# Optimization experiments

Measured on AMD Instinct MI355X. Metric: run time of the kernel, lower is better.

## Reference

```python
import jax, jax.numpy as jnp
import numpy as np

NUM_HEADS = 8
OUT_DIM = 32


def setup_inputs() -> dict:
    key = jax.random.key(0)
    k1, k2, k3, k4 = jax.random.split(key, 4)
    B, N, IN = 2048, 64, 256
    h_i_list = jax.random.normal(k1, (B, N, IN), dtype=jnp.float32)
    h_j_list = jax.random.normal(k2, (B, N, IN), dtype=jnp.float32)
    # Linear weight, applied as x @ W (in_dim, num_heads*out_dim)
    W = jax.random.normal(k3, (IN, NUM_HEADS * OUT_DIM), dtype=jnp.float32) * (1.0 / np.sqrt(IN))
    W_att = jax.random.normal(k4, (1, NUM_HEADS, OUT_DIM), dtype=jnp.float32) * 0.1
    return {"h_i_list": h_i_list, "h_j_list": h_j_list, "W": W, "W_att": W_att}


def reference(h_i_list, h_j_list, W, W_att):
    B, N, _ = h_i_list.shape
    H, D = NUM_HEADS, OUT_DIM
    # [B, N, H, D]
    proj_neigh = (h_j_list @ W).reshape(B, N, H, D)
    proj_self = (h_i_list @ W).reshape(B, N, H, D)
    # attention logits: leakyReLU(sum over feature dim) -> [B, N, H]
    e_ij = jax.nn.leaky_relu(((proj_neigh + proj_self) * W_att[None]).sum(-1), 0.2)
    # softmax over neighbor dim (dim=1)
    alpha = jax.nn.softmax(e_ij, axis=1)  # [B, N, H]
    # weighted neighbor sum -> [B, H, D]
    weight_sum = jnp.einsum("bnh,bnhd->bhd", alpha, proj_neigh)
    # concat=True: [B, 1, H*D]
    h_new = weight_sum.reshape(B, 1, H * D)
    return jax.nn.elu(h_new)
```

## Files before the change

### kernel.cpp

```cpp
#include <hip/hip_runtime.h>

#define NN 64
#define IND 256
#define NH 8
#define OD 32

__device__ __forceinline__ unsigned f2bf(float f) {
  unsigned u = __float_as_uint(f);
  return (u + (((u >> 16) & 1u) + 0x7fffu)) >> 16;
}
__device__ __forceinline__ float bflo(unsigned u) { return __uint_as_float(u << 16); }
__device__ __forceinline__ float bfhi(unsigned u) { return __uint_as_float(u & 0xffff0000u); }

__global__ __launch_bounds__(256) void precompute_v(
    const float* __restrict__ W, const float* __restrict__ Watt, float* __restrict__ V) {
  int tid = blockIdx.x * 256 + threadIdx.x;
  if (tid >= IND * NH) return;
  int h = tid >> 8, k = tid & 255;
  float acc = 0.f;
#pragma unroll
  for (int d = 0; d < OD; ++d) acc += W[k * 256 + h * OD + d] * Watt[h * OD + d];
  V[h * 256 + k] = acc;
}

#define V_OFF 33792
#define E_OFF (33792 + 8320)
#define M_OFF (33792 + 8320 + 2048)
#define SMEM_BYTES (33792 + 8320 + 2048 + 64)

__global__ __launch_bounds__(256) void gat_fused(
    const float* __restrict__ Xi, const float* __restrict__ Xj,
    const float* __restrict__ W, const float* __restrict__ V,
    float* __restrict__ out) {
  __shared__ __align__(16) unsigned char smem[SMEM_BYTES];
  unsigned* s_pk = (unsigned*)smem;
  float* v_f = (float*)(smem + V_OFF);
  float* e_f = (float*)(smem + E_OFF);
  float* m_f = (float*)(smem + M_OFF);
  float* r_f = m_f + 8;
  float* yp_f = (float*)smem;
  float* y_f = (float*)(smem + V_OFF);

  const int t = threadIdx.x;
  const int b = blockIdx.x;
  const int w = t >> 6, l = t & 63;
  const float4* Xi4 = (const float4*)Xi + (size_t)b * (NN * IND / 4);
  const float4* Xj4 = (const float4*)Xj + (size_t)b * (NN * IND / 4);

#pragma unroll
  for (int r = 0; r < 8; ++r) v_f[r * 260 + t] = V[r * 256 + t];

  float4 xj[16];
#pragma unroll
  for (int i = 0; i < 16; ++i) {
    int f4 = i * 256 + t;
    float4 a = Xj4[f4];
    float4 c = Xi4[f4];
    xj[i] = a;
    float sx = a.x + c.x, sy = a.y + c.y, sz = a.z + c.z, sw = a.w + c.w;
    int n = i * 4 + w;
    unsigned p0 = f2bf(sx) | (f2bf(sy) << 16);
    unsigned p1 = f2bf(sz) | (f2bf(sw) << 16);
    *(uint2*)(s_pk + n * 132 + l * 2) = make_uint2(p0, p1);
  }
  __syncthreads();

#pragma unroll
  for (int pp = 0; pp < 2; ++pp) {
    int p = t + pp * 256;
    int n = p >> 3, h = p & 7;
    const uint4* srow = (const uint4*)(s_pk + n * 132);
    const float4* vrow = (const float4*)(v_f + h * 260);
    float acc = 0.f;
#pragma unroll 8
    for (int kk = 0; kk < 32; ++kk) {
      uint4 sp = srow[kk];
      float4 va = vrow[2 * kk], vb = vrow[2 * kk + 1];
      acc += bflo(sp.x) * va.x + bfhi(sp.x) * va.y + bflo(sp.y) * va.z + bfhi(sp.y) * va.w
           + bflo(sp.z) * vb.x + bfhi(sp.z) * vb.y + bflo(sp.w) * vb.z + bfhi(sp.w) * vb.w;
    }
    e_f[p] = acc >= 0.f ? acc : 0.2f * acc;
  }
  __syncthreads();

  if (t < 64) {
    int h = t & 7, g = t >> 3;
    float m = -3.4e38f;
#pragma unroll
    for (int q = 0; q < 8; ++q) m = fmaxf(m, e_f[(g * 8 + q) * 8 + h]);
    m = fmaxf(m, __shfl_xor(m, 8, 64));
    m = fmaxf(m, __shfl_xor(m, 16, 64));
    m = fmaxf(m, __shfl_xor(m, 32, 64));
    float s = 0.f;
#pragma unroll
    for (int q = 0; q < 8; ++q) s += __expf(e_f[(g * 8 + q) * 8 + h] - m);
    s += __shfl_xor(s, 8, 64);
    s += __shfl_xor(s, 16, 64);
    s += __shfl_xor(s, 32, 64);
    if (g == 0) { m_f[h] = m; r_f[h] = 1.f / s; }
  }
  __syncthreads();

#pragma unroll
  for (int pp = 0; pp < 2; ++pp) {
    int p = t + pp * 256;
    int h = p & 7;
    e_f[p] = __expf(e_f[p] - m_f[h]) * r_f[h];
  }
  __syncthreads();

  float4 acc4[8];
#pragma unroll
  for (int h = 0; h < 8; ++h) acc4[h] = make_float4(0.f, 0.f, 0.f, 0.f);
#pragma unroll
  for (int i = 0; i < 16; ++i) {
    int n = i * 4 + w;
    float4 a0 = *(const float4*)(e_f + n * 8);
    float4 a1 = *(const float4*)(e_f + n * 8 + 4);
    float al[8] = {a0.x, a0.y, a0.z, a0.w, a1.x, a1.y, a1.z, a1.w};
    float4 x = xj[i];
#pragma unroll
    for (int h = 0; h < 8; ++h) {
      acc4[h].x += al[h] * x.x;
      acc4[h].y += al[h] * x.y;
      acc4[h].z += al[h] * x.z;
      acc4[h].w += al[h] * x.w;
    }
  }
#pragma unroll
  for (int h = 0; h < 8; ++h)
    *(float4*)(yp_f + (w * 8 + h) * 256 + l * 4) = acc4[h];
  __syncthreads();

#pragma unroll
  for (int r = 0; r < 8; ++r) {
    float y = yp_f[r * 256 + t] + yp_f[(8 + r) * 256 + t] +
              yp_f[(16 + r) * 256 + t] + yp_f[(24 + r) * 256 + t];
    y_f[r * 258 + t] = y;
  }
  __syncthreads();

  {
    int h = t >> 5;
    const float* yrow = y_f + h * 258;
    float acc = 0.f;
#pragma unroll 8
    for (int k = 0; k < 256; ++k) acc += yrow[k] * W[k * 256 + t];
    out[(size_t)b * 256 + t] = acc > 0.f ? acc : (__expf(acc) - 1.f);
  }
}

extern "C" void kernel_launch(void* const* d_in, const int* in_sizes, int n_in,
                              void* d_out, int out_size, void* d_ws, size_t ws_size,
                              hipStream_t stream) {
  const float* Xi = (const float*)d_in[0];
  const float* Xj = (const float*)d_in[1];
  const float* W = (const float*)d_in[2];
  const float* Watt = (const float*)d_in[3];
  float* out = (float*)d_out;
  float* V = (float*)d_ws;
  int B = in_sizes[0] / (NN * IND);
  precompute_v<<<(IND * NH + 255) / 256, 256, 0, stream>>>(W, Watt, V);
  gat_fused<<<B, 256, 0, stream>>>(Xi, Xj, W, V, out);
}
```

Measured before the change: 322.2 us.

## Restructure GAT fused kernel to cut barriers and split the output projection

Each wave now owns a contiguous block of 16 neighbor rows. All Xi/Xj float4 loads are issued before any packing, and the softmax statistics are computed redundantly in every wave with shuffles, which removes the m/r shared-memory stage and two block barriers. The final W projection is split along K across waves, using float4 W loads and a fused partial-sum reduction. A minimum-blocks hint of 3 is added to launch_bounds. Holding xi in registers raises register pressure, and the occupancy hint may force spills.

```diff
diff --git a/kernel.cpp b/kernel.cpp
--- a/kernel.cpp
+++ b/kernel.cpp
@@ -24,11 +24,10 @@
 }
 
 #define V_OFF 33792
-#define E_OFF (33792 + 8320)
-#define M_OFF (33792 + 8320 + 2048)
-#define SMEM_BYTES (33792 + 8320 + 2048 + 64)
+#define E_OFF (V_OFF + 8320)
+#define SMEM_BYTES (E_OFF + 2048)
 
-__global__ __launch_bounds__(256) void gat_fused(
+__global__ __launch_bounds__(256, 3) void gat_fused(
     const float* __restrict__ Xi, const float* __restrict__ Xj,
     const float* __restrict__ W, const float* __restrict__ V,
     float* __restrict__ out) {
@@ -36,39 +35,45 @@
   unsigned* s_pk = (unsigned*)smem;
   float* v_f = (float*)(smem + V_OFF);
   float* e_f = (float*)(smem + E_OFF);
-  float* m_f = (float*)(smem + M_OFF);
-  float* r_f = m_f + 8;
+  float* alpha_f = v_f;
+  float* pp_f = v_f;
   float* yp_f = (float*)smem;
-  float* y_f = (float*)(smem + V_OFF);
 
   const int t = threadIdx.x;
   const int b = blockIdx.x;
   const int w = t >> 6, l = t & 63;
-  const float4* Xi4 = (const float4*)Xi + (size_t)b * (NN * IND / 4);
-  const float4* Xj4 = (const float4*)Xj + (size_t)b * (NN * IND / 4);
+  const int g = l >> 3, h = l & 7;
 
+  const float4* Xi4 = (const float4*)Xi + (size_t)b * (NN * IND / 4) + w * 1024;
+  const float4* Xj4 = (const float4*)Xj + (size_t)b * (NN * IND / 4) + w * 1024;
+
+  {
+    const float4* V4 = (const float4*)V;
+    float4 vs[8];
 #pragma unroll
-  for (int r = 0; r < 8; ++r) v_f[r * 260 + t] = V[r * 256 + t];
+    for (int r = 0; r < 8; ++r) vs[r] = V4[r * 64 + l];
+#pragma unroll
+    for (int r = 0; r < 8; ++r) *(float4*)(v_f + r * 260 + 4 * l) = vs[r];
+  }
 
-  float4 xj[16];
+  float4 xj[16], xi[16];
 #pragma unroll
   for (int i = 0; i < 16; ++i) {
-    int f4 = i * 256 + t;
-    float4 a = Xj4[f4];
-    float4 c = Xi4[f4];
-    xj[i] = a;
-    float sx = a.x + c.x, sy = a.y + c.y, sz = a.z + c.z, sw = a.w + c.w;
-    int n = i * 4 + w;
-    unsigned p0 = f2bf(sx) | (f2bf(sy) << 16);
-    unsigned p1 = f2bf(sz) | (f2bf(sw) << 16);
-    *(uint2*)(s_pk + n * 132 + l * 2) = make_uint2(p0, p1);
+    xj[i] = Xj4[i * 64 + l];
+    xi[i] = Xi4[i * 64 + l];
   }
-  __syncthreads();
+#pragma unroll
+  for (int i = 0; i < 16; ++i) {
+    float4 a = xj[i], c = xi[i];
+    unsigned p0 = f2bf(a.x + c.x) | (f2bf(a.y + c.y) << 16);
+    unsigned p1 = f2bf(a.z + c.z) | (f2bf(a.w + c.w) << 16);
+    *(uint2*)(s_pk + (w * 16 + i) * 132 + l * 2) = make_uint2(p0, p1);
+  }
 
+  float er[2];
 #pragma unroll
   for (int pp = 0; pp < 2; ++pp) {
-    int p = t + pp * 256;
-    int n = p >> 3, h = p & 7;
+    int n = w * 16 + g + 8 * pp;
     const uint4* srow = (const uint4*)(s_pk + n * 132);
     const float4* vrow = (const float4*)(v_f + h * 260);
     float acc = 0.f;
@@ -79,74 +84,76 @@
       acc += bflo(sp.x) * va.x + bfhi(sp.x) * va.y + bflo(sp.y) * va.z + bfhi(sp.y) * va.w
            + bflo(sp.z) * vb.x + bfhi(sp.z) * vb.y + bflo(sp.w) * vb.z + bfhi(sp.w) * vb.w;
     }
-    e_f[p] = acc >= 0.f ? acc : 0.2f * acc;
+    er[pp] = acc >= 0.f ? acc : 0.2f * acc;
+    e_f[n * 8 + h] = er[pp];
   }
   __syncthreads();
 
-  if (t < 64) {
-    int h = t & 7, g = t >> 3;
-    float m = -3.4e38f;
+  float m = -3.4e38f;
 #pragma unroll
-    for (int q = 0; q < 8; ++q) m = fmaxf(m, e_f[(g * 8 + q) * 8 + h]);
-    m = fmaxf(m, __shfl_xor(m, 8, 64));
-    m = fmaxf(m, __shfl_xor(m, 16, 64));
-    m = fmaxf(m, __shfl_xor(m, 32, 64));
-    float s = 0.f;
+  for (int q = 0; q < 8; ++q) m = fmaxf(m, e_f[(g * 8 + q) * 8 + h]);
+  m = fmaxf(m, __shfl_xor(m, 8, 64));
+  m = fmaxf(m, __shfl_xor(m, 16, 64));
+  m = fmaxf(m, __shfl_xor(m, 32, 64));
+  float ssum = 0.f;
 #pragma unroll
-    for (int q = 0; q < 8; ++q) s += __expf(e_f[(g * 8 + q) * 8 + h] - m);
-    s += __shfl_xor(s, 8, 64);
-    s += __shfl_xor(s, 16, 64);
-    s += __shfl_xor(s, 32, 64);
-    if (g == 0) { m_f[h] = m; r_f[h] = 1.f / s; }
-  }
-  __syncthreads();
+  for (int q = 0; q < 8; ++q) ssum += __expf(e_f[(g * 8 + q) * 8 + h] - m);
+  ssum += __shfl_xor(ssum, 8, 64);
+  ssum += __shfl_xor(ssum, 16, 64);
+  ssum += __shfl_xor(ssum, 32, 64);
+  float rinv = 1.f / ssum;
 
 #pragma unroll
   for (int pp = 0; pp < 2; ++pp) {
-    int p = t + pp * 256;
-    int h = p & 7;
-    e_f[p] = __expf(e_f[p] - m_f[h]) * r_f[h];
+    int n = w * 16 + g + 8 * pp;
+    alpha_f[n * 8 + h] = __expf(er[pp] - m) * rinv;
   }
-  __syncthreads();
 
   float4 acc4[8];
 #pragma unroll
-  for (int h = 0; h < 8; ++h) acc4[h] = make_float4(0.f, 0.f, 0.f, 0.f);
+  for (int hh = 0; hh < 8; ++hh) acc4[hh] = make_float4(0.f, 0.f, 0.f, 0.f);
 #pragma unroll
   for (int i = 0; i < 16; ++i) {
-    int n = i * 4 + w;
-    float4 a0 = *(const float4*)(e_f + n * 8);
-    float4 a1 = *(const float4*)(e_f + n * 8 + 4);
+    int n = w * 16 + i;
+    float4 a0 = *(const float4*)(alpha_f + n * 8);
+    float4 a1 = *(const float4*)(alpha_f + n * 8 + 4);
     float al[8] = {a0.x, a0.y, a0.z, a0.w, a1.x, a1.y, a1.z, a1.w};
     float4 x = xj[i];
 #pragma unroll
-    for (int h = 0; h < 8; ++h) {
-      acc4[h].x += al[h] * x.x;
-      acc4[h].y += al[h] * x.y;
-      acc4[h].z += al[h] * x.z;
-      acc4[h].w += al[h] * x.w;
+    for (int hh = 0; hh < 8; ++hh) {
+      acc4[hh].x += al[hh] * x.x;
+      acc4[hh].y += al[hh] * x.y;
+      acc4[hh].z += al[hh] * x.z;
+      acc4[hh].w += al[hh] * x.w;
     }
   }
 #pragma unroll
-  for (int h = 0; h < 8; ++h)
-    *(float4*)(yp_f + (w * 8 + h) * 256 + l * 4) = acc4[h];
+  for (int hh = 0; hh < 8; ++hh)
+    *(float4*)(yp_f + (w * 8 + hh) * 260 + 4 * l) = acc4[hh];
   __syncthreads();
 
-#pragma unroll
-  for (int r = 0; r < 8; ++r) {
-    float y = yp_f[r * 256 + t] + yp_f[(8 + r) * 256 + t] +
-              yp_f[(16 + r) * 256 + t] + yp_f[(24 + r) * 256 + t];
-    y_f[r * 258 + t] = y;
+  {
+    const float* ypb = yp_f + g * 260;
+    const float4* W4 = (const float4*)W;
+    float4 acc = make_float4(0.f, 0.f, 0.f, 0.f);
+    int k0 = w * 64;
+#pragma unroll 8
+    for (int kk = 0; kk < 64; ++kk) {
+      int k = k0 + kk;
+      float yv = ypb[k] + ypb[2080 + k] + ypb[4160 + k] + ypb[6240 + k];
+      float4 wv = W4[k * 64 + l];
+      acc.x += yv * wv.x;
+      acc.y += yv * wv.y;
+      acc.z += yv * wv.z;
+      acc.w += yv * wv.w;
+    }
+    *(float4*)(pp_f + w * 256 + 4 * l) = acc;
   }
   __syncthreads();
 
   {
-    int h = t >> 5;
-    const float* yrow = y_f + h * 258;
-    float acc = 0.f;
-#pragma unroll 8
-    for (int k = 0; k < 256; ++k) acc += yrow[k] * W[k * 256 + t];
-    out[(size_t)b * 256 + t] = acc > 0.f ? acc : (__expf(acc) - 1.f);
+    float s = pp_f[t] + pp_f[256 + t] + pp_f[512 + t] + pp_f[768 + t];
+    out[(size_t)b * 256 + t] = s > 0.f ? s : (__expf(s) - 1.f);
   }
 }
 
```

New measurement: 304.9 us. -5.4%, faster.
